# Kernel tuning notes

Hardware: AMD Instinct MI355X
Metric: run time of the kernel (lower is better)

Reference implementation:

```python
import jax, jax.numpy as jnp
import numpy as np

N_NODES = 100000
N_EDGES = 3200000
N_GRAPHS = 256
NEG_SLOPE = 0.2  # PyG GATConv default


def setup_inputs() -> dict:
    key = jax.random.key(0)
    ks = jax.random.split(key, 20)
    x = jax.random.normal(ks[0], (N_NODES, 20), jnp.float32)
    edge_index = jax.random.randint(ks[1], (2, N_EDGES), 0, N_NODES, dtype=jnp.int32)
    batch = jnp.sort(jax.random.randint(ks[2], (N_NODES,), 0, N_GRAPHS, dtype=jnp.int32))
    s = 0.1
    return {
        "x": x,
        "edge_index": edge_index,
        "batch": batch,
        "num_graphs": N_GRAPHS,
        "w_gat": jax.random.normal(ks[3], (20, 4, 16), jnp.float32) * s,
        "att_src": jax.random.normal(ks[4], (4, 16), jnp.float32) * s,
        "att_dst": jax.random.normal(ks[5], (4, 16), jnp.float32) * s,
        "b_gat": jax.random.normal(ks[6], (64,), jnp.float32) * s,
        "w_fuse": jax.random.normal(ks[7], (64, 64), jnp.float32) * s,
        "b_fuse": jax.random.normal(ks[8], (64,), jnp.float32) * s,
        "w_h1": jax.random.normal(ks[9], (64, 32), jnp.float32) * s,
        "b_h1": jax.random.normal(ks[10], (32,), jnp.float32) * s,
        "w_h2": jax.random.normal(ks[11], (32, 16), jnp.float32) * s,
        "b_h2": jax.random.normal(ks[12], (16,), jnp.float32) * s,
        "w_h3": jax.random.normal(ks[13], (16, 16), jnp.float32) * s,
        "b_h3": jax.random.normal(ks[14], (16,), jnp.float32) * s,
        "w_ev": jax.random.normal(ks[15], (16, 3), jnp.float32) * s,
        "b_ev": jax.random.normal(ks[16], (3,), jnp.float32) * s,
        "w_env": jax.random.normal(ks[17], (16, 3), jnp.float32) * s,
        "b_env": jax.random.normal(ks[18], (3,), jnp.float32) * s,
    }


def gat_conv(x, edge_index, w_gat, att_src, att_dst, b_gat, num_nodes):
    # Linear projection per head: [N, H, C]
    xh = jnp.einsum('nf,fhc->nhc', x, w_gat)
    # add self loops (PyG add_self_loops=True)
    loop = jnp.arange(num_nodes, dtype=edge_index.dtype)
    src = jnp.concatenate([edge_index[0], loop])  # source j
    dst = jnp.concatenate([edge_index[1], loop])  # target i
    # per-node attention terms [N, H]
    a_s = jnp.einsum('nhc,hc->nh', xh, att_src)
    a_d = jnp.einsum('nhc,hc->nh', xh, att_dst)
    # per-edge logit, leaky relu
    logit = jax.nn.leaky_relu(a_s[src] + a_d[dst], NEG_SLOPE)  # [E, H]
    # segment softmax over destination node
    m = jax.ops.segment_max(logit, dst, num_segments=num_nodes)
    e = jnp.exp(logit - m[dst])
    z = jax.ops.segment_sum(e, dst, num_segments=num_nodes)
    alpha = e / z[dst]  # [E, H]
    # weighted scatter-aggregate of source features
    msg = xh[src] * alpha[:, :, None]  # [E, H, C]
    out = jax.ops.segment_sum(msg, dst, num_segments=num_nodes)  # [N, H, C]
    return out.reshape(num_nodes, -1) + b_gat  # concat heads + bias


def reference(x, edge_index, batch, num_graphs, w_gat, att_src, att_dst, b_gat,
              w_fuse, b_fuse, w_h1, b_h1, w_h2, b_h2, w_h3, b_h3,
              w_ev, b_ev, w_env, b_env):
    n = x.shape[0]
    h = gat_conv(x, edge_index, w_gat, att_src, att_dst, b_gat, n)
    h = jax.nn.relu(h @ w_fuse + b_fuse)
    h = jax.nn.relu(h @ w_h1 + b_h1)
    h = jax.nn.relu(h @ w_h2 + b_h2)
    h = jax.nn.relu(h @ w_h3 + b_h3)
    # global mean pool over graphs
    sums = jax.ops.segment_sum(h, batch, num_segments=num_graphs)
    cnts = jax.ops.segment_sum(jnp.ones((n, 1), h.dtype), batch, num_segments=num_graphs)
    g = sums / jnp.maximum(cnts, 1.0)
    out_event = g @ w_ev + b_ev
    out_env = g @ w_env + b_env
    return (out_event, out_env)
```

## Files before the change

kernel.cpp:

```cpp
#include <hip/hip_runtime.h>
#include <hip/hip_bf16.h>
#include <hip/hip_fp16.h>

#define FIN 20
#define HEADS 4
#define F 64
#define NEG_SLOPE 0.2f
#define AP 68
#define BSHIFT 8
#define BMASK 255
#define NVX 8
#define BCAPX 1408
#define MAXBUCK 512
#define BIN_EPT 16

__global__ void __launch_bounds__(256)
prep_bin(const float* __restrict__ x,
         const float* __restrict__ w_gat,
         const float* __restrict__ att_src,
         const float* __restrict__ att_dst,
         __half* __restrict__ xh,
         float* __restrict__ a_s,
         float* __restrict__ a_d,
         const int* __restrict__ ei, int E, int nbuck,
         int* __restrict__ gcount, int* __restrict__ bucketData,
         int n_nodes, int nbP)
{
    if (blockIdx.x < nbP) {
        __shared__ __align__(16) float w[FIN * F];
        __shared__ float asrc[F];
        __shared__ float adst[F];
        for (int i = threadIdx.x; i < FIN * F; i += 256) w[i] = w_gat[i];
        if (threadIdx.x < F) {
            asrc[threadIdx.x] = att_src[threadIdx.x];
            adst[threadIdx.x] = att_dst[threadIdx.x];
        }
        __syncthreads();

        int n = blockIdx.x * 256 + threadIdx.x;
        if (n >= n_nodes) return;

        float xv[FIN];
#pragma unroll
        for (int q = 0; q < FIN / 4; ++q) {
            float4 x4 = *(const float4*)&x[(size_t)n * FIN + q * 4];
            xv[q * 4 + 0] = x4.x; xv[q * 4 + 1] = x4.y;
            xv[q * 4 + 2] = x4.z; xv[q * 4 + 3] = x4.w;
        }

        float as[HEADS] = {0.f, 0.f, 0.f, 0.f};
        float ad[HEADS] = {0.f, 0.f, 0.f, 0.f};

#pragma unroll
        for (int j4 = 0; j4 < F / 4; ++j4) {
            float4 acc = make_float4(0.f, 0.f, 0.f, 0.f);
#pragma unroll
            for (int k = 0; k < FIN; ++k) {
                float4 w4 = *(const float4*)&w[k * F + j4 * 4];
                acc.x += xv[k] * w4.x;
                acc.y += xv[k] * w4.y;
                acc.z += xv[k] * w4.z;
                acc.w += xv[k] * w4.w;
            }
            __half2 p0 = __floats2half2_rn(acc.x, acc.y);
            __half2 p1 = __floats2half2_rn(acc.z, acc.w);
            float2 st;
            ((__half2*)&st)[0] = p0;
            ((__half2*)&st)[1] = p1;
            *(float2*)&xh[(size_t)n * F + j4 * 4] = st;

            int h = j4 >> 2;
            int jb = j4 * 4;
            as[h] += acc.x * asrc[jb] + acc.y * asrc[jb + 1] + acc.z * asrc[jb + 2] + acc.w * asrc[jb + 3];
            ad[h] += acc.x * adst[jb] + acc.y * adst[jb + 1] + acc.z * adst[jb + 2] + acc.w * adst[jb + 3];
        }
#pragma unroll
        for (int h = 0; h < HEADS; ++h) {
            a_s[(size_t)n * HEADS + h] = as[h];
            a_d[(size_t)n * HEADS + h] = ad[h];
        }
    } else {
        __shared__ int lcnt[MAXBUCK];
        __shared__ int lbase[MAXBUCK];
        for (int i = threadIdx.x; i < nbuck; i += 256) lcnt[i] = 0;
        __syncthreads();

        const int bb = blockIdx.x - nbP;
        const int vx = bb & (NVX - 1);
        int* __restrict__ gc = gcount + vx * nbuck;
        int* __restrict__ bdat = bucketData + (size_t)vx * nbuck * BCAPX;

        int base = bb * (256 * BIN_EPT);
        int b_[BIN_EPT], w_[BIN_EPT];
#pragma unroll
        for (int j = 0; j < BIN_EPT; ++j) {
            int e = base + j * 256 + threadIdx.x;
            if (e < E) {
                int src = ei[e];
                int dst = ei[E + e];
                b_[j] = dst >> BSHIFT;
                w_[j] = ((dst & BMASK) << 17) | src;
                atomicAdd(&lcnt[b_[j]], 1);
            } else b_[j] = -1;
        }
        __syncthreads();
        for (int i = threadIdx.x; i < nbuck; i += 256) {
            int c = lcnt[i];
            lbase[i] = c ? atomicAdd(&gc[i], c) : 0;
            lcnt[i] = 0;
        }
        __syncthreads();
#pragma unroll
        for (int j = 0; j < BIN_EPT; ++j) {
            if (b_[j] >= 0) {
                int p = lbase[b_[j]] + atomicAdd(&lcnt[b_[j]], 1);
                if (p < BCAPX) bdat[(size_t)b_[j] * BCAPX + p] = w_[j];
            }
        }
    }
}

__global__ void __launch_bounds__(1024)
csr_build(const int* __restrict__ bucketData, const int* __restrict__ gcount,
          int* __restrict__ off, int* __restrict__ srcs,
          int n_nodes, int total_edges, int nbuck)
{
    __shared__ int hist[256];
    __shared__ int psum[256];
    int b = blockIdx.x;
    int t = threadIdx.x;
    int node0 = b << BSHIFT;
    int nnode = n_nodes - node0; if (nnode > 256) nnode = 256;

    if (t < 256) {
        int acc = 0;
        for (int i = t; i < b; i += 256) {
            int s = 0;
#pragma unroll
            for (int seg = 0; seg < NVX; ++seg) {
                int c = gcount[seg * nbuck + i];
                s += c < BCAPX ? c : BCAPX;
            }
            acc += s;
        }
        psum[t] = acc;
    }
    __syncthreads();
    for (int d = 128; d > 0; d >>= 1) {
        if (t < d) psum[t] += psum[t + d];
        __syncthreads();
    }
    int base = psum[0] + node0;
    __syncthreads();
    if (b == 0 && t == 0) off[n_nodes] = total_edges;

    if (t < 256) hist[t] = 0;
    __syncthreads();
#pragma unroll
    for (int seg = 0; seg < NVX; ++seg) {
        int cntS = gcount[seg * nbuck + b]; cntS = cntS < BCAPX ? cntS : BCAPX;
        const int* bd = bucketData + ((size_t)seg * nbuck + b) * BCAPX;
        for (int i = t; i < cntS; i += 1024) atomicAdd(&hist[bd[i] >> 17], 1);
    }
    __syncthreads();

    if (t < 256) psum[t] = (t < nnode) ? hist[t] + 1 : 0;
    __syncthreads();
    for (int d = 1; d < 256; d <<= 1) {
        int w = (t >= d && t < 256) ? psum[t - d] : 0;
        __syncthreads();
        if (t < 256) psum[t] += w;
        __syncthreads();
    }
    int ex = (t == 0 || t >= 256) ? 0 : psum[t - 1];
    __syncthreads();
    if (t < nnode) {
        int o = base + ex;
        off[node0 + t] = o;
        srcs[o] = node0 + t;
        hist[t] = o + 1;
    }
    __syncthreads();
#pragma unroll
    for (int seg = 0; seg < NVX; ++seg) {
        int cntS = gcount[seg * nbuck + b]; cntS = cntS < BCAPX ? cntS : BCAPX;
        const int* bd = bucketData + ((size_t)seg * nbuck + b) * BCAPX;
        for (int i = t; i < cntS; i += 1024) {
            int w = bd[i];
            int p = atomicAdd(&hist[w >> 17], 1);
            srcs[p] = w & 0x1FFFF;
        }
    }
}

__global__ void __launch_bounds__(256, 4)
gat_mlp(const int* __restrict__ off,
        const int* __restrict__ srcs,
        const float* __restrict__ a_s,
        const float* __restrict__ a_d,
        const __half* __restrict__ xh,
        const float* __restrict__ b_gat,
        const float* __restrict__ w_fuse, const float* __restrict__ b_fuse,
        const float* __restrict__ w_h1, const float* __restrict__ b_h1,
        const float* __restrict__ w_h2, const float* __restrict__ b_h2,
        const float* __restrict__ w_h3, const float* __restrict__ b_h3,
        float* __restrict__ rfeat,
        int n_nodes)
{
    __shared__ __align__(16) __half wfh[64 * 64];
    __shared__ __align__(16) __half w1h[64 * 32];
    __shared__ __align__(16) float w2[32 * 16];
    __shared__ __align__(16) float w3[16 * 16];
    __shared__ __align__(16) float bf[64];
    __shared__ __align__(16) float b1[32], b2[16], b3[16];
    __shared__ __align__(16) float act[32 * AP];

    for (int i = threadIdx.x; i < 64 * 64; i += 256) wfh[i] = __float2half(w_fuse[i]);
    for (int i = threadIdx.x; i < 64 * 32; i += 256) w1h[i] = __float2half(w_h1[i]);
    for (int i = threadIdx.x; i < 32 * 16; i += 256) w2[i] = w_h2[i];
    for (int i = threadIdx.x; i < 16 * 16; i += 256) w3[i] = w_h3[i];
    if (threadIdx.x < 64) bf[threadIdx.x] = b_fuse[threadIdx.x];
    else if (threadIdx.x < 96)  b1[threadIdx.x - 64] = b_h1[threadIdx.x - 64];
    else if (threadIdx.x < 112) b2[threadIdx.x - 96] = b_h2[threadIdx.x - 96];
    else if (threadIdx.x < 128) b3[threadIdx.x - 112] = b_h3[threadIdx.x - 112];

    {
        const int node_l2 = threadIdx.x >> 3;
        const int part = threadIdx.x & 7;
        const int n = blockIdx.x * 32 + node_l2;
        const int h = part >> 1;
        const int g8 = (threadIdx.x & 63) >> 3;

        float acc[8] = {0.f, 0.f, 0.f, 0.f, 0.f, 0.f, 0.f, 0.f};
        float zacc = 0.f;
        bool active = (n < n_nodes);
        if (active) {
            int kb = off[n];
            int ke = off[n + 1];
            float adh = a_d[n * 4 + h];

            int i0 = kb + part;          i0 = i0 < ke - 1 ? i0 : ke - 1;
            int sA = srcs[i0];
            int i1 = kb + 8 + part;      i1 = i1 < ke - 1 ? i1 : ke - 1;
            int sNxt = srcs[i1];

            int sj[8];
#pragma unroll
            for (int j = 0; j < 8; ++j) sj[j] = __shfl(sA, g8 * 8 + j, 64);
            float4 rawA[8]; float aslA[8];
#pragma unroll
            for (int j = 0; j < 8; ++j) {
                rawA[j] = *(const float4*)&xh[(size_t)sj[j] * F + part * 8];
                aslA[j] = a_s[sj[j] * 4 + h];
            }

            float4 rawB[8]; float aslB[8];
            int base = kb;
            while (true) {
                bool hasB = (base + 8 < ke);
                if (hasB) {
#pragma unroll
                    for (int j = 0; j < 8; ++j) sj[j] = __shfl(sNxt, g8 * 8 + j, 64);
#pragma unroll
                    for (int j = 0; j < 8; ++j) {
                        rawB[j] = *(const float4*)&xh[(size_t)sj[j] * F + part * 8];
                        aslB[j] = a_s[sj[j] * 4 + h];
                    }
                    int i2 = base + 16 + part;  i2 = i2 < ke - 1 ? i2 : ke - 1;
                    sNxt = srcs[i2];
                }
#pragma unroll
                for (int j = 0; j < 8; ++j) {
                    float l = aslA[j] + adh;
                    l = l > 0.f ? l : NEG_SLOPE * l;
                    float e = (base + j < ke) ? __expf(l) : 0.f;
                    zacc += e;
                    const __half2* hp = (const __half2*)&rawA[j];
                    float2 c0 = __half22float2(hp[0]);
                    float2 c1 = __half22float2(hp[1]);
                    float2 c2 = __half22float2(hp[2]);
                    float2 c3 = __half22float2(hp[3]);
                    acc[0] += e * c0.x; acc[1] += e * c0.y;
                    acc[2] += e * c1.x; acc[3] += e * c1.y;
                    acc[4] += e * c2.x; acc[5] += e * c2.y;
                    acc[6] += e * c3.x; acc[7] += e * c3.y;
                }
                base += 8;
                if (!hasB) break;

                bool hasC = (base + 8 < ke);
                if (hasC) {
#pragma unroll
                    for (int j = 0; j < 8; ++j) sj[j] = __shfl(sNxt, g8 * 8 + j, 64);
#pragma unroll
                    for (int j = 0; j < 8; ++j) {
                        rawA[j] = *(const float4*)&xh[(size_t)sj[j] * F + part * 8];
                        aslA[j] = a_s[sj[j] * 4 + h];
                    }
                    int i2 = base + 16 + part;  i2 = i2 < ke - 1 ? i2 : ke - 1;
                    sNxt = srcs[i2];
                }
#pragma unroll
                for (int j = 0; j < 8; ++j) {
                    float l = aslB[j] + adh;
                    l = l > 0.f ? l : NEG_SLOPE * l;
                    float e = (base + j < ke) ? __expf(l) : 0.f;
                    zacc += e;
                    const __half2* hp = (const __half2*)&rawB[j];
                    float2 c0 = __half22float2(hp[0]);
                    float2 c1 = __half22float2(hp[1]);
                    float2 c2 = __half22float2(hp[2]);
                    float2 c3 = __half22float2(hp[3]);
                    acc[0] += e * c0.x; acc[1] += e * c0.y;
                    acc[2] += e * c1.x; acc[3] += e * c1.y;
                    acc[4] += e * c2.x; acc[5] += e * c2.y;
                    acc[6] += e * c3.x; acc[7] += e * c3.y;
                }
                base += 8;
                if (!hasC) break;
            }
        }
        float inv = active ? (1.f / zacc) : 0.f;
        float4 bg0 = *(const float4*)&b_gat[part * 8];
        float4 bg1 = *(const float4*)&b_gat[part * 8 + 4];
        float4 o0, o1;
        o0.x = acc[0] * inv + bg0.x; o0.y = acc[1] * inv + bg0.y;
        o0.z = acc[2] * inv + bg0.z; o0.w = acc[3] * inv + bg0.w;
        o1.x = acc[4] * inv + bg1.x; o1.y = acc[5] * inv + bg1.y;
        o1.z = acc[6] * inv + bg1.z; o1.w = acc[7] * inv + bg1.w;
        *(float4*)&act[node_l2 * AP + part * 8]     = o0;
        *(float4*)&act[node_l2 * AP + part * 8 + 4] = o1;
    }
    __syncthreads();

    const int node_l = threadIdx.x >> 4;
    const int part   = threadIdx.x & 15;
    const int nA     = blockIdx.x * 32 + node_l;
    const int nB     = nA + 16;
    const bool actvA = (nA < n_nodes);
    const bool actvB = (nB < n_nodes);

    float* rowA = &act[node_l * AP];
    float* rowB = &act[(node_l + 16) * AP];

    {
        float4 aA = *(const float4*)&bf[part * 4];
        float4 aB = aA;
#pragma unroll
        for (int k4 = 0; k4 < 16; ++k4) {
            float4 hA = *(const float4*)&rowA[k4 * 4];
            float4 hB = *(const float4*)&rowB[k4 * 4];
#pragma unroll
            for (int q = 0; q < 4; ++q) {
                const __half2* wp = (const __half2*)&wfh[(k4 * 4 + q) * 64 + part * 4];
                float2 wlo = __half22float2(wp[0]);
                float2 whi = __half22float2(wp[1]);
                float hva = (q == 0) ? hA.x : (q == 1) ? hA.y : (q == 2) ? hA.z : hA.w;
                float hvb = (q == 0) ? hB.x : (q == 1) ? hB.y : (q == 2) ? hB.z : hB.w;
                aA.x += hva * wlo.x; aA.y += hva * wlo.y;
                aA.z += hva * whi.x; aA.w += hva * whi.y;
                aB.x += hvb * wlo.x; aB.y += hvb * wlo.y;
                aB.z += hvb * whi.x; aB.w += hvb * whi.y;
            }
        }
        aA.x = aA.x > 0.f ? aA.x : 0.f; aA.y = aA.y > 0.f ? aA.y : 0.f;
        aA.z = aA.z > 0.f ? aA.z : 0.f; aA.w = aA.w > 0.f ? aA.w : 0.f;
        aB.x = aB.x > 0.f ? aB.x : 0.f; aB.y = aB.y > 0.f ? aB.y : 0.f;
        aB.z = aB.z > 0.f ? aB.z : 0.f; aB.w = aB.w > 0.f ? aB.w : 0.f;
        *(float4*)&rowA[part * 4] = aA;
        *(float4*)&rowB[part * 4] = aB;
    }

    {
        float axA = b1[part * 2], ayA = b1[part * 2 + 1];
        float axB = axA, ayB = ayA;
#pragma unroll
        for (int k4 = 0; k4 < 16; ++k4) {
            float4 hA = *(const float4*)&rowA[k4 * 4];
            float4 hB = *(const float4*)&rowB[k4 * 4];
#pragma unroll
            for (int q = 0; q < 4; ++q) {
                float2 w2f = __half22float2(*(const __half2*)&w1h[(k4 * 4 + q) * 32 + part * 2]);
                float hva = (q == 0) ? hA.x : (q == 1) ? hA.y : (q == 2) ? hA.z : hA.w;
                float hvb = (q == 0) ? hB.x : (q == 1) ? hB.y : (q == 2) ? hB.z : hB.w;
                axA += hva * w2f.x; ayA += hva * w2f.y;
                axB += hvb * w2f.x; ayB += hvb * w2f.y;
            }
        }
        axA = axA > 0.f ? axA : 0.f; ayA = ayA > 0.f ? ayA : 0.f;
        axB = axB > 0.f ? axB : 0.f; ayB = ayB > 0.f ? ayB : 0.f;
        float2 uA; uA.x = axA; uA.y = ayA;
        float2 uB; uB.x = axB; uB.y = ayB;
        *(float2*)&rowA[part * 2] = uA;
        *(float2*)&rowB[part * 2] = uB;
    }

    {
        float aA = b2[part], aB = aA;
#pragma unroll
        for (int k4 = 0; k4 < 8; ++k4) {
            float4 hA = *(const float4*)&rowA[k4 * 4];
            float4 hB = *(const float4*)&rowB[k4 * 4];
            float w0 = w2[(k4 * 4 + 0) * 16 + part];
            float wq1 = w2[(k4 * 4 + 1) * 16 + part];
            float wq2 = w2[(k4 * 4 + 2) * 16 + part];
            float wq3 = w2[(k4 * 4 + 3) * 16 + part];
            aA += hA.x * w0 + hA.y * wq1 + hA.z * wq2 + hA.w * wq3;
            aB += hB.x * w0 + hB.y * wq1 + hB.z * wq2 + hB.w * wq3;
        }
        aA = aA > 0.f ? aA : 0.f;
        aB = aB > 0.f ? aB : 0.f;
        rowA[part] = aA;
        rowB[part] = aB;
    }

    float rA, rB;
    {
        float aA = b3[part], aB = aA;
#pragma unroll
        for (int k4 = 0; k4 < 4; ++k4) {
            float4 hA = *(const float4*)&rowA[k4 * 4];
            float4 hB = *(const float4*)&rowB[k4 * 4];
            float w0 = w3[(k4 * 4 + 0) * 16 + part];
            float wq1 = w3[(k4 * 4 + 1) * 16 + part];
            float wq2 = w3[(k4 * 4 + 2) * 16 + part];
            float wq3 = w3[(k4 * 4 + 3) * 16 + part];
            aA += hA.x * w0 + hA.y * wq1 + hA.z * wq2 + hA.w * wq3;
            aB += hB.x * w0 + hB.y * wq1 + hB.z * wq2 + hB.w * wq3;
        }
        rA = aA > 0.f ? aA : 0.f;
        rB = aB > 0.f ? aB : 0.f;
    }

    if (actvA) rfeat[(size_t)nA * 16 + part] = rA;
    if (actvB) rfeat[(size_t)nB * 16 + part] = rB;
}

__global__ void __launch_bounds__(256)
pool_head(const float* __restrict__ rfeat, const int* __restrict__ batch,
          const float* __restrict__ w_ev, const float* __restrict__ b_ev,
          const float* __restrict__ w_env, const float* __restrict__ b_env,
          float* __restrict__ out, int n_nodes, int n_graphs)
{
    __shared__ int s_bounds[2];
    __shared__ float partial[16][17];
    __shared__ float gvec[16];

    int g = blockIdx.x;
    if (threadIdx.x < 2) {
        int target = g + threadIdx.x;
        int lo = 0, hi = n_nodes;
        while (lo < hi) { int m = (lo + hi) >> 1; if (batch[m] < target) lo = m + 1; else hi = m; }
        s_bounds[threadIdx.x] = lo;
    }
    __syncthreads();
    int start = s_bounds[0], end = s_bounds[1];

    const int c = threadIdx.x & 15;
    const int w = threadIdx.x >> 4;
    float acc = 0.f;
    for (int i = start + w; i < end; i += 16)
        acc += rfeat[(size_t)i * 16 + c];
    partial[w][c] = acc;
    __syncthreads();

    if (threadIdx.x < 16) {
        float s = 0.f;
#pragma unroll
        for (int ww = 0; ww < 16; ++ww) s += partial[ww][threadIdx.x];
        float cnt = (float)(end - start);
        cnt = cnt > 1.f ? cnt : 1.f;
        gvec[threadIdx.x] = s / cnt;
    }
    __syncthreads();

    if (threadIdx.x < 3) {
        int j = threadIdx.x;
        float a = b_ev[j];
#pragma unroll
        for (int k = 0; k < 16; ++k) a += gvec[k] * w_ev[k * 3 + j];
        out[(size_t)g * 3 + j] = a;
    } else if (threadIdx.x < 6) {
        int j = threadIdx.x - 3;
        float a = b_env[j];
#pragma unroll
        for (int k = 0; k < 16; ++k) a += gvec[k] * w_env[k * 3 + j];
        out[(size_t)n_graphs * 3 + (size_t)g * 3 + j] = a;
    }
}

extern "C" void kernel_launch(void* const* d_in, const int* in_sizes, int n_in,
                              void* d_out, int out_size, void* d_ws, size_t ws_size,
                              hipStream_t stream)
{
    const float* x       = (const float*)d_in[0];
    const int*   ei      = (const int*)d_in[1];
    const int*   batch   = (const int*)d_in[2];
    const float* w_gat   = (const float*)d_in[4];
    const float* att_src = (const float*)d_in[5];
    const float* att_dst = (const float*)d_in[6];
    const float* b_gat   = (const float*)d_in[7];
    const float* w_fuse  = (const float*)d_in[8];
    const float* b_fuse  = (const float*)d_in[9];
    const float* w_h1    = (const float*)d_in[10];
    const float* b_h1    = (const float*)d_in[11];
    const float* w_h2    = (const float*)d_in[12];
    const float* b_h2    = (const float*)d_in[13];
    const float* w_h3    = (const float*)d_in[14];
    const float* b_h3    = (const float*)d_in[15];
    const float* w_ev    = (const float*)d_in[16];
    const float* b_ev    = (const float*)d_in[17];
    const float* w_env   = (const float*)d_in[18];
    const float* b_env   = (const float*)d_in[19];

    const int n_nodes  = in_sizes[0] / FIN;
    const int E        = in_sizes[1] / 2;
    const int n_graphs = 256;
    const int total    = E + n_nodes;
    const int nbuck    = (n_nodes + BMASK) >> BSHIFT;

    float* ws     = (float*)d_ws;
    __half* xh    = (__half*)ws;
    float* a_s    = ws   + (size_t)n_nodes * 32;
    float* a_d    = a_s  + (size_t)n_nodes * HEADS;
    float* rfeat  = a_d  + (size_t)n_nodes * HEADS;
    int*   off    = (int*)(rfeat + (size_t)n_nodes * 16);
    int*   srcs   = off    + n_nodes + 1;
    int*   gcount = srcs   + total;
    int*   bucketData = gcount + NVX * nbuck;

    hipMemsetAsync(gcount, 0, (size_t)NVX * nbuck * sizeof(int), stream);

    const int nbP = (n_nodes + 255) / 256;
    const int nbB = (E + 256 * BIN_EPT - 1) / (256 * BIN_EPT);

    prep_bin<<<nbP + nbB, 256, 0, stream>>>(
        x, w_gat, att_src, att_dst, xh, a_s, a_d,
        ei, E, nbuck, gcount, bucketData, n_nodes, nbP);

    csr_build<<<nbuck, 1024, 0, stream>>>(
        bucketData, gcount, off, srcs, n_nodes, total, nbuck);

    gat_mlp<<<(n_nodes + 31) / 32, 256, 0, stream>>>(
        off, srcs, a_s, a_d, xh, b_gat,
        w_fuse, b_fuse, w_h1, b_h1, w_h2, b_h2, w_h3, b_h3,
        rfeat, n_nodes);

    pool_head<<<n_graphs, 256, 0, stream>>>(
        rfeat, batch, w_ev, b_ev, w_env, b_env, (float*)d_out, n_nodes, n_graphs);
}
```

Baseline: 255.9 us.

## Fuse mean-pool partial sums into GAT-MLP kernel and reuse local atomic ranks

Each GAT-MLP block now reduces its 32 nodes' final features per graph and atomically adds them into a per-graph sum buffer. This removes the rfeat round trip to global memory and the pooling pass, leaving a small head kernel. The binning and CSR-build kernels keep the rank returned by the first shared-memory atomic and reuse it, so the second atomic pass and the re-read of bucket data are dropped. Risks: float atomics make summation order nondeterministic, and csr_build now assumes at most 2048 entries per bucket segment, which holds because BCAPX is 1408.

```diff
diff --git a/kernel.cpp b/kernel.cpp
--- a/kernel.cpp
+++ b/kernel.cpp
@@ -91,7 +91,7 @@
         int* __restrict__ bdat = bucketData + (size_t)vx * nbuck * BCAPX;
 
         int base = bb * (256 * BIN_EPT);
-        int b_[BIN_EPT], w_[BIN_EPT];
+        int b_[BIN_EPT], w_[BIN_EPT], r_[BIN_EPT];
 #pragma unroll
         for (int j = 0; j < BIN_EPT; ++j) {
             int e = base + j * 256 + threadIdx.x;
@@ -100,20 +100,19 @@
                 int dst = ei[E + e];
                 b_[j] = dst >> BSHIFT;
                 w_[j] = ((dst & BMASK) << 17) | src;
-                atomicAdd(&lcnt[b_[j]], 1);
+                r_[j] = atomicAdd(&lcnt[b_[j]], 1);
             } else b_[j] = -1;
         }
         __syncthreads();
         for (int i = threadIdx.x; i < nbuck; i += 256) {
             int c = lcnt[i];
             lbase[i] = c ? atomicAdd(&gc[i], c) : 0;
-            lcnt[i] = 0;
         }
         __syncthreads();
 #pragma unroll
         for (int j = 0; j < BIN_EPT; ++j) {
             if (b_[j] >= 0) {
-                int p = lbase[b_[j]] + atomicAdd(&lcnt[b_[j]], 1);
+                int p = lbase[b_[j]] + r_[j];
                 if (p < BCAPX) bdat[(size_t)b_[j] * BCAPX + p] = w_[j];
             }
         }
@@ -156,11 +155,26 @@
 
     if (t < 256) hist[t] = 0;
     __syncthreads();
+
+    int cS[NVX];
+    int wv[NVX * 2];
+    int rk[NVX * 2];
 #pragma unroll
     for (int seg = 0; seg < NVX; ++seg) {
-        int cntS = gcount[seg * nbuck + b]; cntS = cntS < BCAPX ? cntS : BCAPX;
+        int cntS = gcount[seg * nbuck + b]; cS[seg] = cntS < BCAPX ? cntS : BCAPX;
         const int* bd = bucketData + ((size_t)seg * nbuck + b) * BCAPX;
-        for (int i = t; i < cntS; i += 1024) atomicAdd(&hist[bd[i] >> 17], 1);
+        {
+            bool v = t < cS[seg];
+            int w = v ? bd[t] : 0;
+            wv[seg * 2] = w;
+            rk[seg * 2] = v ? atomicAdd(&hist[w >> 17], 1) : 0;
+        }
+        {
+            bool v = (t + 1024) < cS[seg];
+            int w = v ? bd[t + 1024] : 0;
+            wv[seg * 2 + 1] = w;
+            rk[seg * 2 + 1] = v ? atomicAdd(&hist[w >> 17], 1) : 0;
+        }
     }
     __syncthreads();
 
@@ -181,14 +195,16 @@
         hist[t] = o + 1;
     }
     __syncthreads();
+
 #pragma unroll
     for (int seg = 0; seg < NVX; ++seg) {
-        int cntS = gcount[seg * nbuck + b]; cntS = cntS < BCAPX ? cntS : BCAPX;
-        const int* bd = bucketData + ((size_t)seg * nbuck + b) * BCAPX;
-        for (int i = t; i < cntS; i += 1024) {
-            int w = bd[i];
-            int p = atomicAdd(&hist[w >> 17], 1);
-            srcs[p] = w & 0x1FFFF;
+        if (t < cS[seg]) {
+            int w = wv[seg * 2];
+            srcs[hist[w >> 17] + rk[seg * 2]] = w & 0x1FFFF;
+        }
+        if ((t + 1024) < cS[seg]) {
+            int w = wv[seg * 2 + 1];
+            srcs[hist[w >> 17] + rk[seg * 2 + 1]] = w & 0x1FFFF;
         }
     }
 }
@@ -199,12 +215,13 @@
         const float* __restrict__ a_s,
         const float* __restrict__ a_d,
         const __half* __restrict__ xh,
+        const int* __restrict__ batch,
         const float* __restrict__ b_gat,
         const float* __restrict__ w_fuse, const float* __restrict__ b_fuse,
         const float* __restrict__ w_h1, const float* __restrict__ b_h1,
         const float* __restrict__ w_h2, const float* __restrict__ b_h2,
         const float* __restrict__ w_h3, const float* __restrict__ b_h3,
-        float* __restrict__ rfeat,
+        float* __restrict__ gsum,
         int n_nodes)
 {
     __shared__ __align__(16) __half wfh[64 * 64];
@@ -213,6 +230,7 @@
     __shared__ __align__(16) float w3[16 * 16];
     __shared__ __align__(16) float bf[64];
     __shared__ __align__(16) float b1[32], b2[16], b3[16];
+    __shared__ int gids[32];
     __shared__ __align__(16) float act[32 * AP];
 
     for (int i = threadIdx.x; i < 64 * 64; i += 256) wfh[i] = __float2half(w_fuse[i]);
@@ -223,6 +241,10 @@
     else if (threadIdx.x < 96)  b1[threadIdx.x - 64] = b_h1[threadIdx.x - 64];
     else if (threadIdx.x < 112) b2[threadIdx.x - 96] = b_h2[threadIdx.x - 96];
     else if (threadIdx.x < 128) b3[threadIdx.x - 112] = b_h3[threadIdx.x - 112];
+    else if (threadIdx.x >= 224) {
+        int nn = blockIdx.x * 32 + (threadIdx.x - 224);
+        gids[threadIdx.x - 224] = (nn < n_nodes) ? batch[nn] : -1;
+    }
 
     {
         const int node_l2 = threadIdx.x >> 3;
@@ -335,10 +357,6 @@
 
     const int node_l = threadIdx.x >> 4;
     const int part   = threadIdx.x & 15;
-    const int nA     = blockIdx.x * 32 + node_l;
-    const int nB     = nA + 16;
-    const bool actvA = (nA < n_nodes);
-    const bool actvB = (nB < n_nodes);
 
     float* rowA = &act[node_l * AP];
     float* rowB = &act[(node_l + 16) * AP];
@@ -414,7 +432,6 @@
         rowB[part] = aB;
     }
 
-    float rA, rB;
     {
         float aA = b3[part], aB = aA;
 #pragma unroll
@@ -428,22 +445,34 @@
             aA += hA.x * w0 + hA.y * wq1 + hA.z * wq2 + hA.w * wq3;
             aB += hB.x * w0 + hB.y * wq1 + hB.z * wq2 + hB.w * wq3;
         }
-        rA = aA > 0.f ? aA : 0.f;
-        rB = aB > 0.f ? aB : 0.f;
-    }
-
-    if (actvA) rfeat[(size_t)nA * 16 + part] = rA;
-    if (actvB) rfeat[(size_t)nB * 16 + part] = rB;
+        rowA[part] = aA > 0.f ? aA : 0.f;
+        rowB[part] = aB > 0.f ? aB : 0.f;
+    }
+    __syncthreads();
+
+    if (threadIdx.x < 16) {
+        int c = threadIdx.x;
+        float accg = 0.f; int cur = -2;
+#pragma unroll 4
+        for (int r = 0; r < 32; ++r) {
+            int gid = gids[r];
+            if (gid != cur) {
+                if (cur >= 0) atomicAdd(&gsum[cur * 16 + c], accg);
+                accg = 0.f; cur = gid;
+            }
+            if (gid >= 0) accg += act[r * AP + c];
+        }
+        if (cur >= 0) atomicAdd(&gsum[cur * 16 + c], accg);
+    }
 }
 
-__global__ void __launch_bounds__(256)
-pool_head(const float* __restrict__ rfeat, const int* __restrict__ batch,
-          const float* __restrict__ w_ev, const float* __restrict__ b_ev,
-          const float* __restrict__ w_env, const float* __restrict__ b_env,
-          float* __restrict__ out, int n_nodes, int n_graphs)
+__global__ void __launch_bounds__(64)
+head(const float* __restrict__ gsum, const int* __restrict__ batch,
+     const float* __restrict__ w_ev, const float* __restrict__ b_ev,
+     const float* __restrict__ w_env, const float* __restrict__ b_env,
+     float* __restrict__ out, int n_nodes, int n_graphs)
 {
     __shared__ int s_bounds[2];
-    __shared__ float partial[16][17];
     __shared__ float gvec[16];
 
     int g = blockIdx.x;
@@ -454,23 +483,10 @@
         s_bounds[threadIdx.x] = lo;
     }
     __syncthreads();
-    int start = s_bounds[0], end = s_bounds[1];
-
-    const int c = threadIdx.x & 15;
-    const int w = threadIdx.x >> 4;
-    float acc = 0.f;
-    for (int i = start + w; i < end; i += 16)
-        acc += rfeat[(size_t)i * 16 + c];
-    partial[w][c] = acc;
-    __syncthreads();
-
     if (threadIdx.x < 16) {
-        float s = 0.f;
-#pragma unroll
-        for (int ww = 0; ww < 16; ++ww) s += partial[ww][threadIdx.x];
-        float cnt = (float)(end - start);
+        float cnt = (float)(s_bounds[1] - s_bounds[0]);
         cnt = cnt > 1.f ? cnt : 1.f;
-        gvec[threadIdx.x] = s / cnt;
+        gvec[threadIdx.x] = gsum[g * 16 + threadIdx.x] / cnt;
     }
     __syncthreads();
 
@@ -523,13 +539,15 @@
     __half* xh    = (__half*)ws;
     float* a_s    = ws   + (size_t)n_nodes * 32;
     float* a_d    = a_s  + (size_t)n_nodes * HEADS;
-    float* rfeat  = a_d  + (size_t)n_nodes * HEADS;
-    int*   off    = (int*)(rfeat + (size_t)n_nodes * 16);
+    int*   off    = (int*)(a_d + (size_t)n_nodes * HEADS);
     int*   srcs   = off    + n_nodes + 1;
-    int*   gcount = srcs   + total;
+    float* gsum   = (float*)(srcs + total);
+    int*   gcount = (int*)(gsum + n_graphs * 16);
     int*   bucketData = gcount + NVX * nbuck;
 
-    hipMemsetAsync(gcount, 0, (size_t)NVX * nbuck * sizeof(int), stream);
+    hipMemsetAsync(gsum, 0,
+                   ((size_t)n_graphs * 16 + (size_t)NVX * nbuck) * sizeof(int),
+                   stream);
 
     const int nbP = (n_nodes + 255) / 256;
     const int nbB = (E + 256 * BIN_EPT - 1) / (256 * BIN_EPT);
@@ -542,10 +560,10 @@
         bucketData, gcount, off, srcs, n_nodes, total, nbuck);
 
     gat_mlp<<<(n_nodes + 31) / 32, 256, 0, stream>>>(
-        off, srcs, a_s, a_d, xh, b_gat,
+        off, srcs, a_s, a_d, xh, batch, b_gat,
         w_fuse, b_fuse, w_h1, b_h1, w_h2, b_h2, w_h3, b_h3,
-        rfeat, n_nodes);
-
-    pool_head<<<n_graphs, 256, 0, stream>>>(
-        rfeat, batch, w_ev, b_ev, w_env, b_env, (float*)d_out, n_nodes, n_graphs);
+        gsum, n_nodes);
+
+    head<<<n_graphs, 64, 0, stream>>>(
+        gsum, batch, w_ev, b_ev, w_env, b_env, (float*)d_out, n_nodes, n_graphs);
 }
```

Result: no change. 257.6 us (+0.7%).
